# Kernel tuning notes

Hardware: AMD Instinct MI355X
Metric: run time of the kernel (lower is better)

The kernel has to match this reference:

```python
import jax, jax.numpy as jnp
import numpy as np

D = 256; FF = 1024; NH = 8; NL = 4; NP = 4; HD = D // NH
BS = 4; NQ = 300; NK = 17; LQ = NQ * NK
SHAPES = np.array([[92, 92], [46, 46], [23, 23], [12, 12]], dtype=np.int32)  # (H, W) per level
LV = int((SHAPES[:, 0] * SHAPES[:, 1]).sum())  # 11253

PKEYS = ['wa_in_w','wa_in_b','wa_out_w','wa_out_b','ac_in_w','ac_in_b','ac_out_w','ac_out_b',
         'ms_val_w','ms_val_b','ms_off_w','ms_off_b','ms_aw_w','ms_aw_b','ms_out_w','ms_out_b',
         'gate_w','gate_b','gn_g','gn_b','wn_g','wn_b','an_g','an_b',
         'l1_w','l1_b','l2_w','l2_b','n2_g','n2_b']

def _ln(x, g, b, eps=1e-5):
    m = x.mean(-1, keepdims=True)
    v = ((x - m) ** 2).mean(-1, keepdims=True)
    return (x - m) / jnp.sqrt(v + eps) * g + b

def _mha(q, k, v, in_w, in_b, out_w, out_b):
    # torch nn.MultiheadAttention (batch_first) equivalent
    B, L, _ = q.shape
    wq, wk, wv = jnp.split(in_w, 3, 0); bq, bk, bv = jnp.split(in_b, 3, 0)
    qh = (q @ wq.T + bq).reshape(B, L, NH, HD).transpose(0, 2, 1, 3)
    kh = (k @ wk.T + bk).reshape(B, -1, NH, HD).transpose(0, 2, 1, 3)
    vh = (v @ wv.T + bv).reshape(B, -1, NH, HD).transpose(0, 2, 1, 3)
    scores = jnp.einsum('bhqd,bhkd->bhqk', qh, kh) / jnp.sqrt(jnp.asarray(HD, qh.dtype))
    a = jax.nn.softmax(scores, axis=-1)
    o = jnp.einsum('bhqk,bhkd->bhqd', a, vh).transpose(0, 2, 1, 3).reshape(B, L, D)
    return o @ out_w.T + out_b

def _bilinear(v, loc):
    # v: (bs,H,W,NH,HD); loc: (bs,Lq,NH,P,2) normalized [0,1]. grid_sample bilinear,
    # align_corners=False, zero padding.
    bs, H, W, nh, hd = v.shape
    x = loc[..., 0] * W - 0.5
    y = loc[..., 1] * H - 0.5
    x0 = jnp.floor(x); y0 = jnp.floor(y)
    wx = x - x0; wy = y - y0
    x0i = x0.astype(jnp.int32); y0i = y0.astype(jnp.int32)
    v_flat = v.reshape(bs, H * W, nh, hd)
    Lq, P = loc.shape[1], loc.shape[3]
    def corner(xi, yi):
        valid = ((xi >= 0) & (xi < W) & (yi >= 0) & (yi < H)).astype(v.dtype)
        idx = jnp.clip(yi, 0, H - 1) * W + jnp.clip(xi, 0, W - 1)  # (bs,Lq,NH,P)
        idx2 = idx.transpose(0, 1, 3, 2).reshape(bs, Lq * P, nh)
        g = jnp.take_along_axis(v_flat, idx2[..., None], axis=1)  # (bs,Lq*P,NH,HD)
        g = g.reshape(bs, Lq, P, nh, hd).transpose(0, 1, 3, 2, 4)
        return g * valid[..., None]
    v00 = corner(x0i, y0i); v01 = corner(x0i + 1, y0i)
    v10 = corner(x0i, y0i + 1); v11 = corner(x0i + 1, y0i + 1)
    return (v00 * ((1 - wx) * (1 - wy))[..., None] + v01 * (wx * (1 - wy))[..., None]
            + v10 * ((1 - wx) * wy)[..., None] + v11 * (wx * wy)[..., None])

def _msda(query, ref, memory, p):
    # standard MSDeformAttn core (fused sample + weight)
    bs, Lq, _ = query.shape
    val = (memory @ p['ms_val_w'].T + p['ms_val_b']).reshape(bs, -1, NH, HD)
    off = (query @ p['ms_off_w'].T + p['ms_off_b']).reshape(bs, Lq, NH, NL, NP, 2)
    aw = jax.nn.softmax((query @ p['ms_aw_w'].T + p['ms_aw_b']).reshape(bs, Lq, NH, NL * NP), -1)
    aw = aw.reshape(bs, Lq, NH, NL, NP)
    norm = jnp.asarray(SHAPES[:, ::-1].copy(), query.dtype)  # (NL,2) -> (W,H)
    loc = ref[:, :, None, :, None, :] + off / norm[None, None, None, :, None, :]
    out = jnp.zeros((bs, Lq, NH, HD), query.dtype)
    start = 0
    for l in range(NL):
        H, W = int(SHAPES[l, 0]), int(SHAPES[l, 1])
        vlev = val[:, start:start + H * W].reshape(bs, H, W, NH, HD); start += H * W
        s = _bilinear(vlev, loc[:, :, :, l])  # (bs,Lq,NH,NP,HD)
        out = out + (s * aw[:, :, :, l, :, None]).sum(3)
    return out.reshape(bs, Lq, D) @ p['ms_out_w'].T + p['ms_out_b']

def _forward(tgt_pose, pos, ref, memory, p):
    bs, nq, nk, d = tgt_pose.shape
    # with_pos_embed mutates tgt_pose in-place in the torch code
    tgt_pose = tgt_pose + pos
    q = tgt_pose.reshape(bs * nq, nk, d)
    t2 = _mha(q, q, q, p['wa_in_w'], p['wa_in_b'], p['wa_out_w'], p['wa_out_b']).reshape(bs, nq, nk, d)
    tgt_pose = _ln(tgt_pose + t2, p['wn_g'], p['wn_b'])
    t = tgt_pose.transpose(0, 2, 1, 3).reshape(bs * nk, nq, d)
    t2 = _mha(t, t, t, p['ac_in_w'], p['ac_in_b'], p['ac_out_w'], p['ac_out_b'])
    t = _ln(t + t2, p['an_g'], p['an_b'])
    tgt_pose = t.reshape(bs, nk, nq, d).transpose(0, 2, 1, 3)
    tgt_pose = tgt_pose + pos  # in-place with_pos_embed before cross attn
    t2 = _msda(tgt_pose.reshape(bs, nq * nk, d), ref, memory, p).reshape(bs, nq, nk, d)
    gi = jnp.concatenate([tgt_pose, t2], -1)
    gates = jax.nn.sigmoid(gi @ p['gate_w'].T + p['gate_b'])
    g1, g2 = jnp.split(gates, 2, -1)
    x = _ln(g1 * tgt_pose + g2 * t2, p['gn_g'], p['gn_b'])
    f = jax.nn.relu(x @ p['l1_w'].T + p['l1_b']) @ p['l2_w'].T + p['l2_b']
    return _ln(x + f, p['n2_g'], p['n2_b'])

def setup_inputs() -> dict:
    key = jax.random.key(0)
    ks = iter(jax.random.split(key, 64))
    s = 0.02
    inp = {
        'tgt_pose': jax.random.normal(next(ks), (BS, NQ, NK, D), jnp.float32),
        'tgt_pose_query_pos': jax.random.normal(next(ks), (BS, NQ, NK, D), jnp.float32),
        'tgt_pose_reference_points': jax.random.uniform(next(ks), (BS, LQ, NL, 2), jnp.float32),
        'memory': jax.random.normal(next(ks), (BS, LV, D), jnp.float32),
        'memory_spatial_shapes': jnp.asarray(SHAPES),
    }
    shapes = {
        'wa_in_w': (3 * D, D), 'wa_in_b': (3 * D,), 'wa_out_w': (D, D), 'wa_out_b': (D,),
        'ac_in_w': (3 * D, D), 'ac_in_b': (3 * D,), 'ac_out_w': (D, D), 'ac_out_b': (D,),
        'ms_val_w': (D, D), 'ms_val_b': (D,),
        'ms_off_w': (NH * NL * NP * 2, D), 'ms_off_b': (NH * NL * NP * 2,),
        'ms_aw_w': (NH * NL * NP, D), 'ms_aw_b': (NH * NL * NP,),
        'ms_out_w': (D, D), 'ms_out_b': (D,),
        'gate_w': (2 * D, 2 * D), 'gate_b': (2 * D,),
        'l1_w': (FF, D), 'l1_b': (FF,), 'l2_w': (D, FF), 'l2_b': (D,),
    }
    for k, sh in shapes.items():
        inp[k] = jax.random.normal(next(ks), sh, jnp.float32) * s
    for k in ['gn_g', 'wn_g', 'an_g', 'n2_g']:
        inp[k] = jnp.ones((D,), jnp.float32)
    for k in ['gn_b', 'wn_b', 'an_b', 'n2_b']:
        inp[k] = jnp.zeros((D,), jnp.float32)
    return inp

def reference(tgt_pose, tgt_pose_query_pos, tgt_pose_reference_points, memory, memory_spatial_shapes,
              wa_in_w, wa_in_b, wa_out_w, wa_out_b, ac_in_w, ac_in_b, ac_out_w, ac_out_b,
              ms_val_w, ms_val_b, ms_off_w, ms_off_b, ms_aw_w, ms_aw_b, ms_out_w, ms_out_b,
              gate_w, gate_b, gn_g, gn_b, wn_g, wn_b, an_g, an_b,
              l1_w, l1_b, l2_w, l2_b, n2_g, n2_b):
    p = dict(wa_in_w=wa_in_w, wa_in_b=wa_in_b, wa_out_w=wa_out_w, wa_out_b=wa_out_b,
             ac_in_w=ac_in_w, ac_in_b=ac_in_b, ac_out_w=ac_out_w, ac_out_b=ac_out_b,
             ms_val_w=ms_val_w, ms_val_b=ms_val_b, ms_off_w=ms_off_w, ms_off_b=ms_off_b,
             ms_aw_w=ms_aw_w, ms_aw_b=ms_aw_b, ms_out_w=ms_out_w, ms_out_b=ms_out_b,
             gate_w=gate_w, gate_b=gate_b, gn_g=gn_g, gn_b=gn_b, wn_g=wn_g, wn_b=wn_b,
             an_g=an_g, an_b=an_b, l1_w=l1_w, l1_b=l1_b, l2_w=l2_w, l2_b=l2_b, n2_g=n2_g, n2_b=n2_b)
    return _forward(tgt_pose, tgt_pose_query_pos, tgt_pose_reference_points, memory, p)
```

## Files before the change

### kernel.cpp

```cpp
#include <hip/hip_runtime.h>
#include <math.h>

#define DD   256
#define NHH  8
#define HDIM 32
#define NLV  4
#define NPT  4
#define BSZ  4
#define NQQ  300
#define NKK  17
#define LQQ  (NQQ*NKK)
#define NROW (BSZ*LQQ)
#define LVV  11253
#define FFD  1024

typedef __attribute__((ext_vector_type(8))) short bf16x8;
typedef __attribute__((ext_vector_type(4))) float f32x4;

__device__ __forceinline__ unsigned short f2bf(float f) {
    unsigned int u = __float_as_uint(f);
    u = u + 0x7FFFu + ((u >> 16) & 1u);
    return (unsigned short)(u >> 16);
}

__global__ __launch_bounds__(256) void k_add(const float4* __restrict__ a,
                                             const float4* __restrict__ b,
                                             float4* __restrict__ o, int n4) {
    int i = blockIdx.x * 256 + threadIdx.x;
    if (i < n4) {
        float4 x = a[i], y = b[i];
        o[i] = make_float4(x.x + y.x, x.y + y.y, x.z + y.z, x.w + y.w);
    }
}

__global__ __launch_bounds__(256) void k_concat(const float4* __restrict__ a,
                                                const float4* __restrict__ b,
                                                float4* __restrict__ o, int rows) {
    int i = blockIdx.x * 256 + threadIdx.x;
    if (i >= rows * 128) return;
    int r = i >> 7, c = i & 127;
    o[i] = (c < 64) ? a[(size_t)r * 64 + c] : b[(size_t)r * 64 + (c - 64)];
}

template<int ACT>
__global__ __launch_bounds__(256) void k_gemm_mfma(const float* __restrict__ A,
                                                   const float* __restrict__ B,
                                                   const float* __restrict__ bias,
                                                   float* __restrict__ C,
                                                   int M, int N, int K) {
    __shared__ unsigned short As[128][40];
    __shared__ unsigned short Bs[128][40];
    int t = threadIdx.x;
    int lane = t & 63, w = t >> 6;
    int l16 = lane & 15, hi = lane >> 4;
    int wr = (w >> 1) << 6;
    int wc = (w & 1) << 6;
    int row0 = blockIdx.x * 128, col0 = blockIdx.y * 128;
    int srow = t >> 2;
    int scol = (t & 3) * 8;

    f32x4 acc[4][4];
    #pragma unroll
    for (int m = 0; m < 4; m++)
        #pragma unroll
        for (int n = 0; n < 4; n++) acc[m][n] = (f32x4){0.f, 0.f, 0.f, 0.f};

    for (int k0 = 0; k0 < K; k0 += 32) {
        #pragma unroll
        for (int half = 0; half < 2; half++) {
            int r = srow + half * 64;
            {
                float v[8];
                int gr = row0 + r;
                if (gr < M) {
                    const float4* p = (const float4*)(A + (size_t)gr * K + k0 + scol);
                    float4 x = p[0], y = p[1];
                    v[0] = x.x; v[1] = x.y; v[2] = x.z; v[3] = x.w;
                    v[4] = y.x; v[5] = y.y; v[6] = y.z; v[7] = y.w;
                } else {
                    #pragma unroll
                    for (int i = 0; i < 8; i++) v[i] = 0.f;
                }
                bf16x8 hh;
                #pragma unroll
                for (int i = 0; i < 8; i++) hh[i] = (short)f2bf(v[i]);
                *(bf16x8*)&As[r][scol] = hh;
            }
            {
                int gb = col0 + r;
                const float4* p = (const float4*)(B + (size_t)gb * K + k0 + scol);
                float4 x = p[0], y = p[1];
                float v[8] = {x.x, x.y, x.z, x.w, y.x, y.y, y.z, y.w};
                bf16x8 hh;
                #pragma unroll
                for (int i = 0; i < 8; i++) hh[i] = (short)f2bf(v[i]);
                *(bf16x8*)&Bs[r][scol] = hh;
            }
        }
        __syncthreads();
        bf16x8 af[4], bfr[4];
        #pragma unroll
        for (int m = 0; m < 4; m++) af[m] = *(const bf16x8*)&As[wr + m * 16 + l16][hi * 8];
        #pragma unroll
        for (int n = 0; n < 4; n++) bfr[n] = *(const bf16x8*)&Bs[wc + n * 16 + l16][hi * 8];
        #pragma unroll
        for (int m = 0; m < 4; m++)
            #pragma unroll
            for (int n = 0; n < 4; n++)
                acc[m][n] = __builtin_amdgcn_mfma_f32_16x16x32_bf16(af[m], bfr[n], acc[m][n], 0, 0, 0);
        __syncthreads();
    }
    #pragma unroll
    for (int n = 0; n < 4; n++) {
        int col = col0 + wc + n * 16 + l16;
        float bv = bias[col];
        #pragma unroll
        for (int m = 0; m < 4; m++) {
            #pragma unroll
            for (int r = 0; r < 4; r++) {
                int row = row0 + wr + m * 16 + (hi << 2) + r;
                if (row < M) {
                    float v = acc[m][n][r] + bv;
                    if (ACT == 1) v = fmaxf(v, 0.f);
                    else if (ACT == 2) v = 1.f / (1.f + __expf(-v));
                    C[(size_t)row * N + col] = v;
                }
            }
        }
    }
}

__global__ __launch_bounds__(256) void k_ln_res(const float* __restrict__ A,
                                                const float* __restrict__ Bp,
                                                const float* __restrict__ g,
                                                const float* __restrict__ be,
                                                float* __restrict__ O, int M) {
    int row = blockIdx.x * 4 + (threadIdx.x >> 6);
    int lane = threadIdx.x & 63;
    if (row >= M) return;
    float4 a = ((const float4*)A)[(size_t)row * 64 + lane];
    float4 b = ((const float4*)Bp)[(size_t)row * 64 + lane];
    float x0 = a.x + b.x, x1 = a.y + b.y, x2 = a.z + b.z, x3 = a.w + b.w;
    float s = x0 + x1 + x2 + x3;
    float sq = x0 * x0 + x1 * x1 + x2 * x2 + x3 * x3;
    #pragma unroll
    for (int o = 32; o; o >>= 1) { s += __shfl_xor(s, o); sq += __shfl_xor(sq, o); }
    float mean = s * (1.f / 256.f);
    float var = sq * (1.f / 256.f) - mean * mean;
    float rs = rsqrtf(var + 1e-5f);
    float4 gg = ((const float4*)g)[lane];
    float4 bb = ((const float4*)be)[lane];
    float4 o4;
    o4.x = (x0 - mean) * rs * gg.x + bb.x;
    o4.y = (x1 - mean) * rs * gg.y + bb.y;
    o4.z = (x2 - mean) * rs * gg.z + bb.z;
    o4.w = (x3 - mean) * rs * gg.w + bb.w;
    ((float4*)O)[(size_t)row * 64 + lane] = o4;
}

__global__ __launch_bounds__(256) void k_ln_gate(const float* __restrict__ G,
                                                 const float* __restrict__ Q,
                                                 const float* __restrict__ T2,
                                                 const float* __restrict__ g,
                                                 const float* __restrict__ be,
                                                 float* __restrict__ O, int M) {
    int row = blockIdx.x * 4 + (threadIdx.x >> 6);
    int lane = threadIdx.x & 63;
    if (row >= M) return;
    float4 g1 = ((const float4*)G)[(size_t)row * 128 + lane];
    float4 g2 = ((const float4*)G)[(size_t)row * 128 + 64 + lane];
    float4 q = ((const float4*)Q)[(size_t)row * 64 + lane];
    float4 t = ((const float4*)T2)[(size_t)row * 64 + lane];
    float x0 = g1.x * q.x + g2.x * t.x;
    float x1 = g1.y * q.y + g2.y * t.y;
    float x2 = g1.z * q.z + g2.z * t.z;
    float x3 = g1.w * q.w + g2.w * t.w;
    float s = x0 + x1 + x2 + x3;
    float sq = x0 * x0 + x1 * x1 + x2 * x2 + x3 * x3;
    #pragma unroll
    for (int o = 32; o; o >>= 1) { s += __shfl_xor(s, o); sq += __shfl_xor(sq, o); }
    float mean = s * (1.f / 256.f);
    float var = sq * (1.f / 256.f) - mean * mean;
    float rs = rsqrtf(var + 1e-5f);
    float4 gg = ((const float4*)g)[lane];
    float4 bb = ((const float4*)be)[lane];
    float4 o4;
    o4.x = (x0 - mean) * rs * gg.x + bb.x;
    o4.y = (x1 - mean) * rs * gg.y + bb.y;
    o4.z = (x2 - mean) * rs * gg.z + bb.z;
    o4.w = (x3 - mean) * rs * gg.w + bb.w;
    ((float4*)O)[(size_t)row * 64 + lane] = o4;
}

__global__ __launch_bounds__(64) void k_wattn(const float* __restrict__ QKV,
                                              float* __restrict__ AO) {
    int unit = blockIdx.x;
    int h = unit & 7;
    int sqc = unit >> 3;
    int lane = threadIdx.x;
    __shared__ float q[17][32], kk[17][32], vv[17][32], sc[17][17];
    for (int idx = lane; idx < 17 * 32; idx += 64) {
        int r = idx >> 5, c = idx & 31;
        const float* base = QKV + (size_t)(sqc * 17 + r) * 768 + h * 32 + c;
        q[r][c] = base[0];
        kk[r][c] = base[256];
        vv[r][c] = base[512];
    }
    __syncthreads();
    const float scale = 0.17677669529663687f;
    for (int idx = lane; idx < 289; idx += 64) {
        int i = idx / 17, j = idx % 17;
        float d = 0.f;
        #pragma unroll
        for (int c = 0; c < 32; c++) d += q[i][c] * kk[j][c];
        sc[i][j] = d * scale;
    }
    __syncthreads();
    if (lane < 17) {
        float mm = -1e30f;
        for (int j = 0; j < 17; j++) mm = fmaxf(mm, sc[lane][j]);
        float ss = 0.f;
        for (int j = 0; j < 17; j++) { float e = __expf(sc[lane][j] - mm); sc[lane][j] = e; ss += e; }
        float iv = 1.f / ss;
        for (int j = 0; j < 17; j++) sc[lane][j] *= iv;
    }
    __syncthreads();
    for (int idx = lane; idx < 17 * 32; idx += 64) {
        int i = idx >> 5, c = idx & 31;
        float o = 0.f;
        #pragma unroll
        for (int j = 0; j < 17; j++) o += sc[i][j] * vv[j][c];
        AO[(size_t)(sqc * 17 + i) * 256 + h * 32 + c] = o;
    }
}

__global__ __launch_bounds__(256) void k_acattn_mfma(const float* __restrict__ QKV,
                                                     float* __restrict__ AO) {
    __shared__ unsigned short Ks[64][40];
    __shared__ unsigned short Vt[32][66];
    __shared__ unsigned short Pl[4][16][72];

    int blk = blockIdx.x;
    int qb = blk % 5;
    int rest = blk / 5;
    int h = rest & 7;
    int bk = rest >> 3;
    int kslot = bk % 17;
    int b = bk / 17;

    int t = threadIdx.x;
    int lane = t & 63, w = t >> 6;
    int l16 = lane & 15, hi = lane >> 4;
    const float scale = 0.17677669529663687f;

    int q0 = qb * 64;
    int qrow = q0 + (w << 4) + l16;
    int qc = qrow < 300 ? qrow : 299;
    bf16x8 qf;
    {
        const float* qp = QKV + ((size_t)(b * 300 + qc) * 17 + kslot) * 768 + h * 32 + hi * 8;
        float4 x = ((const float4*)qp)[0];
        float4 y = ((const float4*)qp)[1];
        float v[8] = {x.x, x.y, x.z, x.w, y.x, y.y, y.z, y.w};
        #pragma unroll
        for (int i = 0; i < 8; i++) qf[i] = (short)f2bf(v[i] * scale);
    }

    f32x4 acc0 = (f32x4){0.f, 0.f, 0.f, 0.f};
    f32x4 acc1 = (f32x4){0.f, 0.f, 0.f, 0.f};
    float m[4], l[4];
    #pragma unroll
    for (int r = 0; r < 4; r++) { m[r] = -1e30f; l[r] = 0.f; }

    int jl = t >> 2;
    int sc = (t & 3) * 8;

    for (int c0 = 0; c0 < 300; c0 += 64) {
        __syncthreads();
        {
            int krow = c0 + jl; if (krow > 299) krow = 299;
            const float* kp = QKV + ((size_t)(b * 300 + krow) * 17 + kslot) * 768 + 256 + h * 32 + sc;
            float4 x = ((const float4*)kp)[0];
            float4 y = ((const float4*)kp)[1];
            float v[8] = {x.x, x.y, x.z, x.w, y.x, y.y, y.z, y.w};
            bf16x8 hK;
            #pragma unroll
            for (int i = 0; i < 8; i++) hK[i] = (short)f2bf(v[i]);
            *(bf16x8*)&Ks[jl][sc] = hK;
            const float* vp = kp + 256;
            float4 vx = ((const float4*)vp)[0];
            float4 vy = ((const float4*)vp)[1];
            float vv[8] = {vx.x, vx.y, vx.z, vx.w, vy.x, vy.y, vy.z, vy.w};
            #pragma unroll
            for (int i = 0; i < 8; i++) Vt[sc + i][jl] = f2bf(vv[i]);
        }
        __syncthreads();

        f32x4 S[4];
        #pragma unroll
        for (int jt = 0; jt < 4; jt++) {
            bf16x8 kf = *(const bf16x8*)&Ks[jt * 16 + l16][hi * 8];
            S[jt] = __builtin_amdgcn_mfma_f32_16x16x32_bf16(qf, kf,
                     (f32x4){0.f, 0.f, 0.f, 0.f}, 0, 0, 0);
        }
        float cm[4] = {-1e30f, -1e30f, -1e30f, -1e30f};
        #pragma unroll
        for (int jt = 0; jt < 4; jt++) {
            bool ok = (c0 + jt * 16 + l16) < 300;
            #pragma unroll
            for (int r = 0; r < 4; r++) {
                float s = ok ? S[jt][r] : -1e30f;
                S[jt][r] = s;
                cm[r] = fmaxf(cm[r], s);
            }
        }
        #pragma unroll
        for (int o = 1; o < 16; o <<= 1)
            #pragma unroll
            for (int r = 0; r < 4; r++) cm[r] = fmaxf(cm[r], __shfl_xor(cm[r], o));
        float corr[4];
        #pragma unroll
        for (int r = 0; r < 4; r++) {
            float nm = fmaxf(m[r], cm[r]);
            corr[r] = __expf(m[r] - nm);
            m[r] = nm;
        }
        float ps[4] = {0.f, 0.f, 0.f, 0.f};
        #pragma unroll
        for (int jt = 0; jt < 4; jt++)
            #pragma unroll
            for (int r = 0; r < 4; r++) {
                float p = __expf(S[jt][r] - m[r]);
                S[jt][r] = p;
                ps[r] += p;
            }
        #pragma unroll
        for (int o = 1; o < 16; o <<= 1)
            #pragma unroll
            for (int r = 0; r < 4; r++) ps[r] += __shfl_xor(ps[r], o);
        #pragma unroll
        for (int r = 0; r < 4; r++) l[r] = l[r] * corr[r] + ps[r];
        #pragma unroll
        for (int r = 0; r < 4; r++) { acc0[r] *= corr[r]; acc1[r] *= corr[r]; }
        #pragma unroll
        for (int jt = 0; jt < 4; jt++)
            #pragma unroll
            for (int r = 0; r < 4; r++)
                Pl[w][(hi << 2) + r][jt * 16 + l16] = f2bf(S[jt][r]);
        #pragma unroll
        for (int half = 0; half < 2; half++) {
            bf16x8 pf = *(const bf16x8*)&Pl[w][l16][half * 32 + hi * 8];
            bf16x8 vf0 = *(const bf16x8*)&Vt[l16][half * 32 + hi * 8];
            bf16x8 vf1 = *(const bf16x8*)&Vt[16 + l16][half * 32 + hi * 8];
            acc0 = __builtin_amdgcn_mfma_f32_16x16x32_bf16(pf, vf0, acc0, 0, 0, 0);
            acc1 = __builtin_amdgcn_mfma_f32_16x16x32_bf16(pf, vf1, acc1, 0, 0, 0);
        }
    }
    #pragma unroll
    for (int r = 0; r < 4; r++) {
        int q = q0 + (w << 4) + (hi << 2) + r;
        if (q < 300) {
            float inv = 1.f / l[r];
            float* op = AO + ((size_t)(b * 300 + q) * 17 + kslot) * 256 + h * 32;
            op[l16] = acc0[r] * inv;
            op[16 + l16] = acc1[r] * inv;
        }
    }
}

__global__ __launch_bounds__(256) void k_msda(const float* __restrict__ OFF,
                                              const float* __restrict__ AWL,
                                              const float* __restrict__ REF,
                                              const float* __restrict__ VAL,
                                              float* __restrict__ OUT) {
    __shared__ int   sIdx[128][4];
    __shared__ float sWgt[128][4];
    const int Hs[4] = {92, 46, 23, 12};
    const int starts[4] = {0, 8464, 10580, 11109};
    int rowq = blockIdx.x;
    int b = rowq / 5100;
    int tid = threadIdx.x;

    if (tid < 128) {
        int h = tid >> 4, p = tid & 15;
        float logit = AWL[(size_t)rowq * 128 + h * 16 + p];
        float mx = logit;
        #pragma unroll
        for (int o = 1; o < 16; o <<= 1) mx = fmaxf(mx, __shfl_xor(mx, o));
        float e = __expf(logit - mx);
        float ssum = e;
        #pragma unroll
        for (int o = 1; o < 16; o <<= 1) ssum += __shfl_xor(ssum, o);
        float aw = e / ssum;

        int l = p >> 2;
        int Ww = Hs[l];
        float fw = (float)Ww;
        float rx = REF[(size_t)rowq * 8 + l * 2];
        float ry = REF[(size_t)rowq * 8 + l * 2 + 1];
        float ox = OFF[(size_t)rowq * 256 + h * 32 + p * 2];
        float oy = OFF[(size_t)rowq * 256 + h * 32 + p * 2 + 1];
        float x = (rx + ox / fw) * fw - 0.5f;
        float y = (ry + oy / fw) * fw - 0.5f;
        float x0f = floorf(x), y0f = floorf(y);
        float wx = x - x0f, wy = y - y0f;
        int x0 = (int)x0f, y0 = (int)y0f;
        bool xv0 = (x0 >= 0) & (x0 < Ww), xv1 = (x0 + 1 >= 0) & (x0 + 1 < Ww);
        bool yv0 = (y0 >= 0) & (y0 < Ww), yv1 = (y0 + 1 >= 0) & (y0 + 1 < Ww);
        int x0c = min(max(x0, 0), Ww - 1), x1c = min(max(x0 + 1, 0), Ww - 1);
        int y0c = min(max(y0, 0), Ww - 1), y1c = min(max(y0 + 1, 0), Ww - 1);
        int base = b * LVV + starts[l];
        sIdx[tid][0] = base + y0c * Ww + x0c;
        sIdx[tid][1] = base + y0c * Ww + x1c;
        sIdx[tid][2] = base + y1c * Ww + x0c;
        sIdx[tid][3] = base + y1c * Ww + x1c;
        sWgt[tid][0] = (yv0 && xv0) ? (1.f - wx) * (1.f - wy) * aw : 0.f;
        sWgt[tid][1] = (yv0 && xv1) ? wx * (1.f - wy) * aw : 0.f;
        sWgt[tid][2] = (yv1 && xv0) ? (1.f - wx) * wy * aw : 0.f;
        sWgt[tid][3] = (yv1 && xv1) ? wx * wy * aw : 0.f;
    }
    __syncthreads();

    int h = tid >> 5, hd = tid & 31;
    int off = h * 32 + hd;
    float out = 0.f;
    #pragma unroll
    for (int p = 0; p < 16; p++) {
        int mI = h * 16 + p;
        int i0 = sIdx[mI][0], i1 = sIdx[mI][1], i2 = sIdx[mI][2], i3 = sIdx[mI][3];
        float w0 = sWgt[mI][0], w1 = sWgt[mI][1], w2 = sWgt[mI][2], w3 = sWgt[mI][3];
        out += w0 * VAL[(size_t)i0 * 256 + off]
             + w1 * VAL[(size_t)i1 * 256 + off]
             + w2 * VAL[(size_t)i2 * 256 + off]
             + w3 * VAL[(size_t)i3 * 256 + off];
    }
    OUT[(size_t)rowq * 256 + off] = out;
}

extern "C" void kernel_launch(void* const* d_in, const int* in_sizes, int n_in,
                              void* d_out, int out_size, void* d_ws, size_t ws_size,
                              hipStream_t stream) {
    const float* tgt     = (const float*)d_in[0];
    const float* pos     = (const float*)d_in[1];
    const float* refpts  = (const float*)d_in[2];
    const float* memory  = (const float*)d_in[3];
    const float* wa_in_w  = (const float*)d_in[5];
    const float* wa_in_b  = (const float*)d_in[6];
    const float* wa_out_w = (const float*)d_in[7];
    const float* wa_out_b = (const float*)d_in[8];
    const float* ac_in_w  = (const float*)d_in[9];
    const float* ac_in_b  = (const float*)d_in[10];
    const float* ac_out_w = (const float*)d_in[11];
    const float* ac_out_b = (const float*)d_in[12];
    const float* ms_val_w = (const float*)d_in[13];
    const float* ms_val_b = (const float*)d_in[14];
    const float* ms_off_w = (const float*)d_in[15];
    const float* ms_off_b = (const float*)d_in[16];
    const float* ms_aw_w  = (const float*)d_in[17];
    const float* ms_aw_b  = (const float*)d_in[18];
    const float* ms_out_w = (const float*)d_in[19];
    const float* ms_out_b = (const float*)d_in[20];
    const float* gate_w   = (const float*)d_in[21];
    const float* gate_b   = (const float*)d_in[22];
    const float* l1_w     = (const float*)d_in[23];
    const float* l1_b     = (const float*)d_in[24];
    const float* l2_w     = (const float*)d_in[25];
    const float* l2_b     = (const float*)d_in[26];
    const float* gn_g     = (const float*)d_in[27];
    const float* wn_g     = (const float*)d_in[28];
    const float* an_g     = (const float*)d_in[29];
    const float* n2_g     = (const float*)d_in[30];
    const float* gn_b     = (const float*)d_in[31];
    const float* wn_b     = (const float*)d_in[32];
    const float* an_b     = (const float*)d_in[33];
    const float* n2_b     = (const float*)d_in[34];

    float* ws = (float*)d_ws;
    const size_t SROW = (size_t)NROW * 256;
    float* TP  = ws;
    float* Qb  = ws + SROW;
    float* T2  = ws + 2 * SROW;
    float* BIG = ws + 3 * SROW;
    float* OFF = BIG;
    float* AW  = BIG + SROW;
    float* VAL = BIG + (size_t)NROW * 384;
    float* GI    = BIG;
    float* GATES = BIG + (size_t)NROW * 512;
    float* Xb  = (float*)d_out;

    const int n4 = NROW * 64;
    const int gx = (NROW + 127) / 128;
    const int gxv = (BSZ * LVV + 127) / 128;

    k_add<<<(n4 + 255) / 256, 256, 0, stream>>>((const float4*)tgt, (const float4*)pos, (float4*)TP, n4);
    k_gemm_mfma<0><<<dim3(gx, 6), 256, 0, stream>>>(TP, wa_in_w, wa_in_b, BIG, NROW, 768, 256);
    k_wattn<<<1200 * 8, 64, 0, stream>>>(BIG, T2);
    k_gemm_mfma<0><<<dim3(gx, 2), 256, 0, stream>>>(T2, wa_out_w, wa_out_b, Xb, NROW, 256, 256);
    k_ln_res<<<(NROW + 3) / 4, 256, 0, stream>>>(TP, Xb, wn_g, wn_b, TP, NROW);
    k_gemm_mfma<0><<<dim3(gx, 6), 256, 0, stream>>>(TP, ac_in_w, ac_in_b, BIG, NROW, 768, 256);
    k_acattn_mfma<<<68 * 8 * 5, 256, 0, stream>>>(BIG, T2);
    k_gemm_mfma<0><<<dim3(gx, 2), 256, 0, stream>>>(T2, ac_out_w, ac_out_b, Xb, NROW, 256, 256);
    k_ln_res<<<(NROW + 3) / 4, 256, 0, stream>>>(TP, Xb, an_g, an_b, TP, NROW);
    k_add<<<(n4 + 255) / 256, 256, 0, stream>>>((const float4*)TP, (const float4*)pos, (float4*)Qb, n4);
    k_gemm_mfma<0><<<dim3(gxv, 2), 256, 0, stream>>>(memory, ms_val_w, ms_val_b, VAL, BSZ * LVV, 256, 256);
    k_gemm_mfma<0><<<dim3(gx, 2), 256, 0, stream>>>(Qb, ms_off_w, ms_off_b, OFF, NROW, 256, 256);
    k_gemm_mfma<0><<<dim3(gx, 1), 256, 0, stream>>>(Qb, ms_aw_w, ms_aw_b, AW, NROW, 128, 256);
    k_msda<<<NROW, 256, 0, stream>>>(OFF, AW, refpts, VAL, TP);
    k_gemm_mfma<0><<<dim3(gx, 2), 256, 0, stream>>>(TP, ms_out_w, ms_out_b, T2, NROW, 256, 256);
    k_concat<<<(NROW * 128 + 255) / 256, 256, 0, stream>>>((const float4*)Qb, (const float4*)T2, (float4*)GI, NROW);
    k_gemm_mfma<2><<<dim3(gx, 4), 256, 0, stream>>>(GI, gate_w, gate_b, GATES, NROW, 512, 512);
    k_ln_gate<<<(NROW + 3) / 4, 256, 0, stream>>>(GATES, Qb, T2, gn_g, gn_b, Xb, NROW);
    k_gemm_mfma<1><<<dim3(gx, 8), 256, 0, stream>>>(Xb, l1_w, l1_b, BIG, NROW, 1024, 256);
    k_gemm_mfma<0><<<dim3(gx, 2), 256, 0, stream>>>(BIG, l2_w, l2_b, T2, NROW, 256, 1024);
    k_ln_res<<<(NROW + 3) / 4, 256, 0, stream>>>(Xb, T2, n2_g, n2_b, (float*)d_out, NROW);
}
```

Baseline: 838.7 us.

## Store intermediate activations and weights in bf16 across the pipeline

Pre-converts all weight matrices to bf16 once per call and switches most intermediate activation buffers (QKV, attention outputs, offsets, values, gates, FFN hidden) to bf16. GEMMs now load bf16 operands directly and can emit bf16 and/or fp32 outputs, and the attention, MSDA and gate-LN kernels read bf16 inputs. This roughly halves memory traffic for intermediates and removes per-tile conversion work inside GEMMs, at the cost of extra rounding of intermediates and a weight conversion kernel per launch.

```diff
diff --git a/kernel.cpp b/kernel.cpp
--- a/kernel.cpp
+++ b/kernel.cpp
@@ -4,17 +4,15 @@
 #define DD   256
 #define NHH  8
 #define HDIM 32
-#define NLV  4
-#define NPT  4
 #define BSZ  4
 #define NQQ  300
 #define NKK  17
 #define LQQ  (NQQ*NKK)
 #define NROW (BSZ*LQQ)
 #define LVV  11253
-#define FFD  1024
 
 typedef __attribute__((ext_vector_type(8))) short bf16x8;
+typedef __attribute__((ext_vector_type(4))) short b16x4;
 typedef __attribute__((ext_vector_type(4))) float f32x4;
 
 __device__ __forceinline__ unsigned short f2bf(float f) {
@@ -22,39 +20,90 @@
     u = u + 0x7FFFu + ((u >> 16) & 1u);
     return (unsigned short)(u >> 16);
 }
-
-__global__ __launch_bounds__(256) void k_add(const float4* __restrict__ a,
-                                             const float4* __restrict__ b,
-                                             float4* __restrict__ o, int n4) {
+__device__ __forceinline__ float b2f(unsigned short u) {
+    return __uint_as_float((unsigned int)u << 16);
+}
+
+__global__ __launch_bounds__(256) void k_wcvt(const float* __restrict__ wa_in, const float* __restrict__ wa_out,
+                                              const float* __restrict__ ac_in, const float* __restrict__ ac_out,
+                                              const float* __restrict__ ms_val, const float* __restrict__ ms_off,
+                                              const float* __restrict__ ms_aw, const float* __restrict__ ms_out,
+                                              const float* __restrict__ gate, const float* __restrict__ l1,
+                                              const float* __restrict__ l2, unsigned short* __restrict__ W16) {
+    size_t idx = ((size_t)blockIdx.x * 256 + threadIdx.x) * 8;
+    if (idx >= 1540096) return;
+    const float* src; size_t loc;
+    if      (idx <  196608) { src = wa_in;  loc = idx; }
+    else if (idx <  262144) { src = wa_out; loc = idx -  196608; }
+    else if (idx <  458752) { src = ac_in;  loc = idx -  262144; }
+    else if (idx <  524288) { src = ac_out; loc = idx -  458752; }
+    else if (idx <  589824) { src = ms_val; loc = idx -  524288; }
+    else if (idx <  655360) { src = ms_off; loc = idx -  589824; }
+    else if (idx <  688128) { src = ms_aw;  loc = idx -  655360; }
+    else if (idx <  753664) { src = ms_out; loc = idx -  688128; }
+    else if (idx < 1015808) { src = gate;   loc = idx -  753664; }
+    else if (idx < 1277952) { src = l1;     loc = idx - 1015808; }
+    else                    { src = l2;     loc = idx - 1277952; }
+    float4 x = ((const float4*)(src + loc))[0];
+    float4 y = ((const float4*)(src + loc))[1];
+    float v[8] = {x.x, x.y, x.z, x.w, y.x, y.y, y.z, y.w};
+    bf16x8 h;
+    #pragma unroll
+    for (int i = 0; i < 8; i++) h[i] = (short)f2bf(v[i]);
+    *(bf16x8*)(W16 + idx) = h;
+}
+
+__global__ __launch_bounds__(256) void k_add_dw(const float4* __restrict__ a, const float4* __restrict__ b,
+                                                float4* __restrict__ o32, unsigned short* __restrict__ o16, int n8) {
     int i = blockIdx.x * 256 + threadIdx.x;
-    if (i < n4) {
-        float4 x = a[i], y = b[i];
-        o[i] = make_float4(x.x + y.x, x.y + y.y, x.z + y.z, x.w + y.w);
-    }
-}
-
-__global__ __launch_bounds__(256) void k_concat(const float4* __restrict__ a,
-                                                const float4* __restrict__ b,
-                                                float4* __restrict__ o, int rows) {
+    if (i >= n8) return;
+    float4 x0 = a[i * 2], y0 = b[i * 2];
+    float4 x1 = a[i * 2 + 1], y1 = b[i * 2 + 1];
+    float4 s0 = make_float4(x0.x + y0.x, x0.y + y0.y, x0.z + y0.z, x0.w + y0.w);
+    float4 s1 = make_float4(x1.x + y1.x, x1.y + y1.y, x1.z + y1.z, x1.w + y1.w);
+    o32[i * 2] = s0; o32[i * 2 + 1] = s1;
+    bf16x8 h;
+    h[0]=(short)f2bf(s0.x); h[1]=(short)f2bf(s0.y); h[2]=(short)f2bf(s0.z); h[3]=(short)f2bf(s0.w);
+    h[4]=(short)f2bf(s1.x); h[5]=(short)f2bf(s1.y); h[6]=(short)f2bf(s1.z); h[7]=(short)f2bf(s1.w);
+    *(bf16x8*)(o16 + (size_t)i * 8) = h;
+}
+
+__global__ __launch_bounds__(256) void k_add_b16(const float4* __restrict__ a, const float4* __restrict__ b,
+                                                 unsigned short* __restrict__ o16, int n8) {
     int i = blockIdx.x * 256 + threadIdx.x;
-    if (i >= rows * 128) return;
-    int r = i >> 7, c = i & 127;
-    o[i] = (c < 64) ? a[(size_t)r * 64 + c] : b[(size_t)r * 64 + (c - 64)];
-}
-
-template<int ACT>
-__global__ __launch_bounds__(256) void k_gemm_mfma(const float* __restrict__ A,
-                                                   const float* __restrict__ B,
+    if (i >= n8) return;
+    float4 x0 = a[i * 2], y0 = b[i * 2];
+    float4 x1 = a[i * 2 + 1], y1 = b[i * 2 + 1];
+    bf16x8 h;
+    h[0]=(short)f2bf(x0.x+y0.x); h[1]=(short)f2bf(x0.y+y0.y); h[2]=(short)f2bf(x0.z+y0.z); h[3]=(short)f2bf(x0.w+y0.w);
+    h[4]=(short)f2bf(x1.x+y1.x); h[5]=(short)f2bf(x1.y+y1.y); h[6]=(short)f2bf(x1.z+y1.z); h[7]=(short)f2bf(x1.w+y1.w);
+    *(bf16x8*)(o16 + (size_t)i * 8) = h;
+}
+
+__global__ __launch_bounds__(256) void k_concat16(const unsigned short* __restrict__ a,
+                                                  const unsigned short* __restrict__ b,
+                                                  unsigned short* __restrict__ o, int rows) {
+    int i = blockIdx.x * 256 + threadIdx.x;
+    if (i >= rows * 64) return;
+    int r = i >> 6, c8 = i & 63;
+    const unsigned short* src = (c8 < 32) ? (a + (size_t)r * 256 + c8 * 8)
+                                          : (b + (size_t)r * 256 + (c8 - 32) * 8);
+    *(bf16x8*)(o + (size_t)r * 512 + c8 * 8) = *(const bf16x8*)src;
+}
+
+template<int ACT, int OMODE, bool A32>
+__global__ __launch_bounds__(256) void k_gemm_mfma(const void* __restrict__ Av,
+                                                   const unsigned short* __restrict__ B,
                                                    const float* __restrict__ bias,
-                                                   float* __restrict__ C,
+                                                   float* __restrict__ C32,
+                                                   unsigned short* __restrict__ C16,
                                                    int M, int N, int K) {
     __shared__ unsigned short As[128][40];
     __shared__ unsigned short Bs[128][40];
     int t = threadIdx.x;
     int lane = t & 63, w = t >> 6;
     int l16 = lane & 15, hi = lane >> 4;
-    int wr = (w >> 1) << 6;
-    int wc = (w & 1) << 6;
+    int wr = (w >> 1) << 6, wc = (w & 1) << 6;
     int row0 = blockIdx.x * 128, col0 = blockIdx.y * 128;
     int srow = t >> 2;
     int scol = (t & 3) * 8;
@@ -69,14 +118,14 @@
         #pragma unroll
         for (int half = 0; half < 2; half++) {
             int r = srow + half * 64;
-            {
+            int gr = row0 + r;
+            if (A32) {
+                const float* A = (const float*)Av;
                 float v[8];
-                int gr = row0 + r;
                 if (gr < M) {
                     const float4* p = (const float4*)(A + (size_t)gr * K + k0 + scol);
                     float4 x = p[0], y = p[1];
-                    v[0] = x.x; v[1] = x.y; v[2] = x.z; v[3] = x.w;
-                    v[4] = y.x; v[5] = y.y; v[6] = y.z; v[7] = y.w;
+                    v[0]=x.x; v[1]=x.y; v[2]=x.z; v[3]=x.w; v[4]=y.x; v[5]=y.y; v[6]=y.z; v[7]=y.w;
                 } else {
                     #pragma unroll
                     for (int i = 0; i < 8; i++) v[i] = 0.f;
@@ -85,17 +134,15 @@
                 #pragma unroll
                 for (int i = 0; i < 8; i++) hh[i] = (short)f2bf(v[i]);
                 *(bf16x8*)&As[r][scol] = hh;
+            } else {
+                const unsigned short* A = (const unsigned short*)Av;
+                bf16x8 hh;
+                if (gr < M) hh = *(const bf16x8*)(A + (size_t)gr * K + k0 + scol);
+                else        hh = (bf16x8){0,0,0,0,0,0,0,0};
+                *(bf16x8*)&As[r][scol] = hh;
             }
-            {
-                int gb = col0 + r;
-                const float4* p = (const float4*)(B + (size_t)gb * K + k0 + scol);
-                float4 x = p[0], y = p[1];
-                float v[8] = {x.x, x.y, x.z, x.w, y.x, y.y, y.z, y.w};
-                bf16x8 hh;
-                #pragma unroll
-                for (int i = 0; i < 8; i++) hh[i] = (short)f2bf(v[i]);
-                *(bf16x8*)&Bs[r][scol] = hh;
-            }
+            int gb = col0 + r;
+            *(bf16x8*)&Bs[r][scol] = *(const bf16x8*)(B + (size_t)gb * K + k0 + scol);
         }
         __syncthreads();
         bf16x8 af[4], bfr[4];
@@ -123,18 +170,21 @@
                     float v = acc[m][n][r] + bv;
                     if (ACT == 1) v = fmaxf(v, 0.f);
                     else if (ACT == 2) v = 1.f / (1.f + __expf(-v));
-                    C[(size_t)row * N + col] = v;
+                    if (OMODE & 1) C32[(size_t)row * N + col] = v;
+                    if (OMODE & 2) C16[(size_t)row * N + col] = f2bf(v);
                 }
             }
         }
     }
 }
 
+template<bool DUAL>
 __global__ __launch_bounds__(256) void k_ln_res(const float* __restrict__ A,
                                                 const float* __restrict__ Bp,
                                                 const float* __restrict__ g,
                                                 const float* __restrict__ be,
-                                                float* __restrict__ O, int M) {
+                                                float* __restrict__ O,
+                                                unsigned short* __restrict__ O16, int M) {
     int row = blockIdx.x * 4 + (threadIdx.x >> 6);
     int lane = threadIdx.x & 63;
     if (row >= M) return;
@@ -156,25 +206,31 @@
     o4.z = (x2 - mean) * rs * gg.z + bb.z;
     o4.w = (x3 - mean) * rs * gg.w + bb.w;
     ((float4*)O)[(size_t)row * 64 + lane] = o4;
-}
-
-__global__ __launch_bounds__(256) void k_ln_gate(const float* __restrict__ G,
-                                                 const float* __restrict__ Q,
-                                                 const float* __restrict__ T2,
-                                                 const float* __restrict__ g,
-                                                 const float* __restrict__ be,
-                                                 float* __restrict__ O, int M) {
+    if (DUAL) {
+        b16x4 h;
+        h[0]=(short)f2bf(o4.x); h[1]=(short)f2bf(o4.y); h[2]=(short)f2bf(o4.z); h[3]=(short)f2bf(o4.w);
+        *(b16x4*)(O16 + (size_t)row * 256 + lane * 4) = h;
+    }
+}
+
+__global__ __launch_bounds__(256) void k_ln_gate_b(const unsigned short* __restrict__ G,
+                                                   const unsigned short* __restrict__ Q,
+                                                   const unsigned short* __restrict__ T2,
+                                                   const float* __restrict__ g,
+                                                   const float* __restrict__ be,
+                                                   float* __restrict__ O,
+                                                   unsigned short* __restrict__ O16, int M) {
     int row = blockIdx.x * 4 + (threadIdx.x >> 6);
     int lane = threadIdx.x & 63;
     if (row >= M) return;
-    float4 g1 = ((const float4*)G)[(size_t)row * 128 + lane];
-    float4 g2 = ((const float4*)G)[(size_t)row * 128 + 64 + lane];
-    float4 q = ((const float4*)Q)[(size_t)row * 64 + lane];
-    float4 t = ((const float4*)T2)[(size_t)row * 64 + lane];
-    float x0 = g1.x * q.x + g2.x * t.x;
-    float x1 = g1.y * q.y + g2.y * t.y;
-    float x2 = g1.z * q.z + g2.z * t.z;
-    float x3 = g1.w * q.w + g2.w * t.w;
+    b16x4 g1 = *(const b16x4*)(G + (size_t)row * 512 + lane * 4);
+    b16x4 g2 = *(const b16x4*)(G + (size_t)row * 512 + 256 + lane * 4);
+    b16x4 q  = *(const b16x4*)(Q + (size_t)row * 256 + lane * 4);
+    b16x4 tt = *(const b16x4*)(T2 + (size_t)row * 256 + lane * 4);
+    float x0 = b2f((unsigned short)g1[0]) * b2f((unsigned short)q[0]) + b2f((unsigned short)g2[0]) * b2f((unsigned short)tt[0]);
+    float x1 = b2f((unsigned short)g1[1]) * b2f((unsigned short)q[1]) + b2f((unsigned short)g2[1]) * b2f((unsigned short)tt[1]);
+    float x2 = b2f((unsigned short)g1[2]) * b2f((unsigned short)q[2]) + b2f((unsigned short)g2[2]) * b2f((unsigned short)tt[2]);
+    float x3 = b2f((unsigned short)g1[3]) * b2f((unsigned short)q[3]) + b2f((unsigned short)g2[3]) * b2f((unsigned short)tt[3]);
     float s = x0 + x1 + x2 + x3;
     float sq = x0 * x0 + x1 * x1 + x2 * x2 + x3 * x3;
     #pragma unroll
@@ -190,10 +246,13 @@
     o4.z = (x2 - mean) * rs * gg.z + bb.z;
     o4.w = (x3 - mean) * rs * gg.w + bb.w;
     ((float4*)O)[(size_t)row * 64 + lane] = o4;
-}
-
-__global__ __launch_bounds__(64) void k_wattn(const float* __restrict__ QKV,
-                                              float* __restrict__ AO) {
+    b16x4 h;
+    h[0]=(short)f2bf(o4.x); h[1]=(short)f2bf(o4.y); h[2]=(short)f2bf(o4.z); h[3]=(short)f2bf(o4.w);
+    *(b16x4*)(O16 + (size_t)row * 256 + lane * 4) = h;
+}
+
+__global__ __launch_bounds__(64) void k_wattn_b(const unsigned short* __restrict__ QKV,
+                                                unsigned short* __restrict__ AO) {
     int unit = blockIdx.x;
     int h = unit & 7;
     int sqc = unit >> 3;
@@ -201,10 +260,10 @@
     __shared__ float q[17][32], kk[17][32], vv[17][32], sc[17][17];
     for (int idx = lane; idx < 17 * 32; idx += 64) {
         int r = idx >> 5, c = idx & 31;
-        const float* base = QKV + (size_t)(sqc * 17 + r) * 768 + h * 32 + c;
-        q[r][c] = base[0];
-        kk[r][c] = base[256];
-        vv[r][c] = base[512];
+        const unsigned short* base = QKV + (size_t)(sqc * 17 + r) * 768 + h * 32 + c;
+        q[r][c] = b2f(base[0]);
+        kk[r][c] = b2f(base[256]);
+        vv[r][c] = b2f(base[512]);
     }
     __syncthreads();
     const float scale = 0.17677669529663687f;
@@ -230,12 +289,12 @@
         float o = 0.f;
         #pragma unroll
         for (int j = 0; j < 17; j++) o += sc[i][j] * vv[j][c];
-        AO[(size_t)(sqc * 17 + i) * 256 + h * 32 + c] = o;
-    }
-}
-
-__global__ __launch_bounds__(256) void k_acattn_mfma(const float* __restrict__ QKV,
-                                                     float* __restrict__ AO) {
+        AO[(size_t)(sqc * 17 + i) * 256 + h * 32 + c] = f2bf(o);
+    }
+}
+
+__global__ __launch_bounds__(256) void k_acattn_mfma_b(const unsigned short* __restrict__ QKV,
+                                                       unsigned short* __restrict__ AO) {
     __shared__ unsigned short Ks[64][40];
     __shared__ unsigned short Vt[32][66];
     __shared__ unsigned short Pl[4][16][72];
@@ -256,15 +315,7 @@
     int q0 = qb * 64;
     int qrow = q0 + (w << 4) + l16;
     int qc = qrow < 300 ? qrow : 299;
-    bf16x8 qf;
-    {
-        const float* qp = QKV + ((size_t)(b * 300 + qc) * 17 + kslot) * 768 + h * 32 + hi * 8;
-        float4 x = ((const float4*)qp)[0];
-        float4 y = ((const float4*)qp)[1];
-        float v[8] = {x.x, x.y, x.z, x.w, y.x, y.y, y.z, y.w};
-        #pragma unroll
-        for (int i = 0; i < 8; i++) qf[i] = (short)f2bf(v[i] * scale);
-    }
+    bf16x8 qf = *(const bf16x8*)(QKV + ((size_t)(b * 300 + qc) * 17 + kslot) * 768 + h * 32 + hi * 8);
 
     f32x4 acc0 = (f32x4){0.f, 0.f, 0.f, 0.f};
     f32x4 acc1 = (f32x4){0.f, 0.f, 0.f, 0.f};
@@ -279,20 +330,11 @@
         __syncthreads();
         {
             int krow = c0 + jl; if (krow > 299) krow = 299;
-            const float* kp = QKV + ((size_t)(b * 300 + krow) * 17 + kslot) * 768 + 256 + h * 32 + sc;
-            float4 x = ((const float4*)kp)[0];
-            float4 y = ((const float4*)kp)[1];
-            float v[8] = {x.x, x.y, x.z, x.w, y.x, y.y, y.z, y.w};
-            bf16x8 hK;
-            #pragma unroll
-            for (int i = 0; i < 8; i++) hK[i] = (short)f2bf(v[i]);
-            *(bf16x8*)&Ks[jl][sc] = hK;
-            const float* vp = kp + 256;
-            float4 vx = ((const float4*)vp)[0];
-            float4 vy = ((const float4*)vp)[1];
-            float vv[8] = {vx.x, vx.y, vx.z, vx.w, vy.x, vy.y, vy.z, vy.w};
-            #pragma unroll
-            for (int i = 0; i < 8; i++) Vt[sc + i][jl] = f2bf(vv[i]);
+            const unsigned short* kp = QKV + ((size_t)(b * 300 + krow) * 17 + kslot) * 768 + 256 + h * 32 + sc;
+            *(bf16x8*)&Ks[jl][sc] = *(const bf16x8*)kp;
+            bf16x8 vv = *(const bf16x8*)(kp + 256);
+            #pragma unroll
+            for (int i = 0; i < 8; i++) Vt[sc + i][jl] = (unsigned short)vv[i];
         }
         __syncthreads();
 
@@ -309,7 +351,7 @@
             bool ok = (c0 + jt * 16 + l16) < 300;
             #pragma unroll
             for (int r = 0; r < 4; r++) {
-                float s = ok ? S[jt][r] : -1e30f;
+                float s = ok ? S[jt][r] * scale : -1e30f;
                 S[jt][r] = s;
                 cm[r] = fmaxf(cm[r], s);
             }
@@ -361,18 +403,18 @@
         int q = q0 + (w << 4) + (hi << 2) + r;
         if (q < 300) {
             float inv = 1.f / l[r];
-            float* op = AO + ((size_t)(b * 300 + q) * 17 + kslot) * 256 + h * 32;
-            op[l16] = acc0[r] * inv;
-            op[16 + l16] = acc1[r] * inv;
-        }
-    }
-}
-
-__global__ __launch_bounds__(256) void k_msda(const float* __restrict__ OFF,
-                                              const float* __restrict__ AWL,
-                                              const float* __restrict__ REF,
-                                              const float* __restrict__ VAL,
-                                              float* __restrict__ OUT) {
+            unsigned short* op = AO + ((size_t)(b * 300 + q) * 17 + kslot) * 256 + h * 32;
+            op[l16] = f2bf(acc0[r] * inv);
+            op[16 + l16] = f2bf(acc1[r] * inv);
+        }
+    }
+}
+
+__global__ __launch_bounds__(256) void k_msda_b(const unsigned short* __restrict__ OFF,
+                                                const unsigned short* __restrict__ AWL,
+                                                const float* __restrict__ REF,
+                                                const unsigned short* __restrict__ VAL,
+                                                unsigned short* __restrict__ OUT) {
     __shared__ int   sIdx[128][4];
     __shared__ float sWgt[128][4];
     const int Hs[4] = {92, 46, 23, 12};
@@ -383,7 +425,7 @@
 
     if (tid < 128) {
         int h = tid >> 4, p = tid & 15;
-        float logit = AWL[(size_t)rowq * 128 + h * 16 + p];
+        float logit = b2f(AWL[(size_t)rowq * 128 + h * 16 + p]);
         float mx = logit;
         #pragma unroll
         for (int o = 1; o < 16; o <<= 1) mx = fmaxf(mx, __shfl_xor(mx, o));
@@ -398,8 +440,8 @@
         float fw = (float)Ww;
         float rx = REF[(size_t)rowq * 8 + l * 2];
         float ry = REF[(size_t)rowq * 8 + l * 2 + 1];
-        float ox = OFF[(size_t)rowq * 256 + h * 32 + p * 2];
-        float oy = OFF[(size_t)rowq * 256 + h * 32 + p * 2 + 1];
+        float ox = b2f(OFF[(size_t)rowq * 256 + h * 32 + p * 2]);
+        float oy = b2f(OFF[(size_t)rowq * 256 + h * 32 + p * 2 + 1]);
         float x = (rx + ox / fw) * fw - 0.5f;
         float y = (ry + oy / fw) * fw - 0.5f;
         float x0f = floorf(x), y0f = floorf(y);
@@ -429,12 +471,12 @@
         int mI = h * 16 + p;
         int i0 = sIdx[mI][0], i1 = sIdx[mI][1], i2 = sIdx[mI][2], i3 = sIdx[mI][3];
         float w0 = sWgt[mI][0], w1 = sWgt[mI][1], w2 = sWgt[mI][2], w3 = sWgt[mI][3];
-        out += w0 * VAL[(size_t)i0 * 256 + off]
-             + w1 * VAL[(size_t)i1 * 256 + off]
-             + w2 * VAL[(size_t)i2 * 256 + off]
-             + w3 * VAL[(size_t)i3 * 256 + off];
-    }
-    OUT[(size_t)rowq * 256 + off] = out;
+        out += w0 * b2f(VAL[(size_t)i0 * 256 + off])
+             + w1 * b2f(VAL[(size_t)i1 * 256 + off])
+             + w2 * b2f(VAL[(size_t)i2 * 256 + off])
+             + w3 * b2f(VAL[(size_t)i3 * 256 + off]);
+    }
+    OUT[(size_t)rowq * 256 + off] = f2bf(out);
 }
 
 extern "C" void kernel_launch(void* const* d_in, const int* in_sizes, int n_in,
@@ -475,42 +517,63 @@
     const float* an_b     = (const float*)d_in[33];
     const float* n2_b     = (const float*)d_in[34];
 
-    float* ws = (float*)d_ws;
-    const size_t SROW = (size_t)NROW * 256;
-    float* TP  = ws;
-    float* Qb  = ws + SROW;
-    float* T2  = ws + 2 * SROW;
-    float* BIG = ws + 3 * SROW;
-    float* OFF = BIG;
-    float* AW  = BIG + SROW;
-    float* VAL = BIG + (size_t)NROW * 384;
-    float* GI    = BIG;
-    float* GATES = BIG + (size_t)NROW * 512;
-    float* Xb  = (float*)d_out;
-
-    const int n4 = NROW * 64;
+    const size_t SROWF = (size_t)NROW * 256;
+    float* TP32 = (float*)d_ws;
+    float* T232 = TP32 + SROWF;
+    unsigned short* us0 = (unsigned short*)(TP32 + 2 * SROWF);
+    unsigned short* OFF16 = us0;
+    unsigned short* AW16  = us0 + 5222400;
+    unsigned short* TP16  = us0 + 7833600;
+    unsigned short* T216  = us0 + 13056000;
+    unsigned short* Qb16  = us0 + 18278400;
+    unsigned short* X16   = us0 + 23500800;
+    unsigned short* W16   = us0 + 28723200;
+    unsigned short* SH    = us0 + 30263296;
+    unsigned short* QKV16  = SH;
+    unsigned short* VAL16  = SH;
+    unsigned short* MS16   = SH + 12000000;
+    unsigned short* GI16   = SH;
+    unsigned short* GATES16= SH + 10444800;
+    unsigned short* F116   = SH;
+    float* Xb32 = (float*)d_out;
+
+    const unsigned short* W_wa_in  = W16;
+    const unsigned short* W_wa_out = W16 + 196608;
+    const unsigned short* W_ac_in  = W16 + 262144;
+    const unsigned short* W_ac_out = W16 + 458752;
+    const unsigned short* W_ms_val = W16 + 524288;
+    const unsigned short* W_ms_off = W16 + 589824;
+    const unsigned short* W_ms_aw  = W16 + 655360;
+    const unsigned short* W_ms_out = W16 + 688128;
+    const unsigned short* W_gate   = W16 + 753664;
+    const unsigned short* W_l1     = W16 + 1015808;
+    const unsigned short* W_l2     = W16 + 1277952;
+
+    const int n8 = NROW * 32;
     const int gx = (NROW + 127) / 128;
     const int gxv = (BSZ * LVV + 127) / 128;
 
-    k_add<<<(n4 + 255) / 256, 256, 0, stream>>>((const float4*)tgt, (const float4*)pos, (float4*)TP, n4);
-    k_gemm_mfma<0><<<dim3(gx, 6), 256, 0, stream>>>(TP, wa_in_w, wa_in_b, BIG, NROW, 768, 256);
-    k_wattn<<<1200 * 8, 64, 0, stream>>>(BIG, T2);
-    k_gemm_mfma<0><<<dim3(gx, 2), 256, 0, stream>>>(T2, wa_out_w, wa_out_b, Xb, NROW, 256, 256);
-    k_ln_res<<<(NROW + 3) / 4, 256, 0, stream>>>(TP, Xb, wn_g, wn_b, TP, NROW);
-    k_gemm_mfma<0><<<dim3(gx, 6), 256, 0, stream>>>(TP, ac_in_w, ac_in_b, BIG, NROW, 768, 256);
-    k_acattn_mfma<<<68 * 8 * 5, 256, 0, stream>>>(BIG, T2);
-    k_gemm_mfma<0><<<dim3(gx, 2), 256, 0, stream>>>(T2, ac_out_w, ac_out_b, Xb, NROW, 256, 256);
-    k_ln_res<<<(NROW + 3) / 4, 256, 0, stream>>>(TP, Xb, an_g, an_b, TP, NROW);
-    k_add<<<(n4 + 255) / 256, 256, 0, stream>>>((const float4*)TP, (const float4*)pos, (float4*)Qb, n4);
-    k_gemm_mfma<0><<<dim3(gxv, 2), 256, 0, stream>>>(memory, ms_val_w, ms_val_b, VAL, BSZ * LVV, 256, 256);
-    k_gemm_mfma<0><<<dim3(gx, 2), 256, 0, stream>>>(Qb, ms_off_w, ms_off_b, OFF, NROW, 256, 256);
-    k_gemm_mfma<0><<<dim3(gx, 1), 256, 0, stream>>>(Qb, ms_aw_w, ms_aw_b, AW, NROW, 128, 256);
-    k_msda<<<NROW, 256, 0, stream>>>(OFF, AW, refpts, VAL, TP);
-    k_gemm_mfma<0><<<dim3(gx, 2), 256, 0, stream>>>(TP, ms_out_w, ms_out_b, T2, NROW, 256, 256);
-    k_concat<<<(NROW * 128 + 255) / 256, 256, 0, stream>>>((const float4*)Qb, (const float4*)T2, (float4*)GI, NROW);
-    k_gemm_mfma<2><<<dim3(gx, 4), 256, 0, stream>>>(GI, gate_w, gate_b, GATES, NROW, 512, 512);
-    k_ln_gate<<<(NROW + 3) / 4, 256, 0, stream>>>(GATES, Qb, T2, gn_g, gn_b, Xb, NROW);
-    k_gemm_mfma<1><<<dim3(gx, 8), 256, 0, stream>>>(Xb, l1_w, l1_b, BIG, NROW, 1024, 256);
-    k_gemm_mfma<0><<<dim3(gx, 2), 256, 0, stream>>>(BIG, l2_w, l2_b, T2, NROW, 256, 1024);
-    k_ln_res<<<(NROW + 3) / 4, 256, 0, stream>>>(Xb, T2, n2_g, n2_b, (float*)d_out, NROW);
-}
+    k_wcvt<<<753, 256, 0, stream>>>(wa_in_w, wa_out_w, ac_in_w, ac_out_w, ms_val_w, ms_off_w,
+                                    ms_aw_w, ms_out_w, gate_w, l1_w, l2_w, W16);
+    k_add_dw<<<(n8 + 255) / 256, 256, 0, stream>>>((const float4*)tgt, (const float4*)pos, (float4*)TP32, TP16, n8);
+    k_gemm_mfma<0, 2, false><<<dim3(gx, 6), 256, 0, stream>>>(TP16, W_wa_in, wa_in_b, nullptr, QKV16, NROW, 768, 256);
+    k_wattn_b<<<1200 * 8, 64, 0, stream>>>(QKV16, T216);
+    k_gemm_mfma<0, 1, false><<<dim3(gx, 2), 256, 0, stream>>>(T216, W_wa_out, wa_out_b, Xb32, nullptr, NROW, 256, 256);
+    k_ln_res<true><<<(NROW + 3) / 4, 256, 0, stream>>>(TP32, Xb32, wn_g, wn_b, TP32, TP16, NROW);
+    k_gemm_mfma<0, 2, false><<<dim3(gx, 6), 256, 0, stream>>>(TP16, W_ac_in, ac_in_b, nullptr, QKV16, NROW, 768, 256);
+    k_acattn_mfma_b<<<68 * 8 * 5, 256, 0, stream>>>(QKV16, T216);
+    k_gemm_mfma<0, 1, false><<<dim3(gx, 2), 256, 0, stream>>>(T216, W_ac_out, ac_out_b, Xb32, nullptr, NROW, 256, 256);
+    k_ln_res<false><<<(NROW + 3) / 4, 256, 0, stream>>>(TP32, Xb32, an_g, an_b, TP32, nullptr, NROW);
+    k_add_b16<<<(n8 + 255) / 256, 256, 0, stream>>>((const float4*)TP32, (const float4*)pos, Qb16, n8);
+    k_gemm_mfma<0, 2, true><<<dim3(gxv, 2), 256, 0, stream>>>(memory, W_ms_val, ms_val_b, nullptr, VAL16, BSZ * LVV, 256, 256);
+    k_gemm_mfma<0, 2, false><<<dim3(gx, 2), 256, 0, stream>>>(Qb16, W_ms_off, ms_off_b, nullptr, OFF16, NROW, 256, 256);
+    k_gemm_mfma<0, 2, false><<<dim3(gx, 1), 256, 0, stream>>>(Qb16, W_ms_aw, ms_aw_b, nullptr, AW16, NROW, 128, 256);
+    k_msda_b<<<NROW, 256, 0, stream>>>(OFF16, AW16, refpts, VAL16, MS16);
+    k_gemm_mfma<0, 2, false><<<dim3(gx, 2), 256, 0, stream>>>(MS16, W_ms_out, ms_out_b, nullptr, T216, NROW, 256, 256);
+    k_concat16<<<(NROW * 64 + 255) / 256, 256, 0, stream>>>(Qb16, T216, GI16, NROW);
+    k_gemm_mfma<2, 2, false><<<dim3(gx, 4), 256, 0, stream>>>(GI16, W_gate, gate_b, nullptr, GATES16, NROW, 512, 512);
+    k_ln_gate_b<<<(NROW + 3) / 4, 256, 0, stream>>>(GATES16, Qb16, T216, gn_g, gn_b, Xb32, X16, NROW);
+    k_gemm_mfma<1, 2, false><<<dim3(gx, 8), 256, 0, stream>>>(X16, W_l1, l1_b, nullptr, F116, NROW, 1024, 256);
+    k_gemm_mfma<0, 1, false><<<dim3(gx, 2), 256, 0, stream>>>(F116, W_l2, l2_b, T232, nullptr, NROW, 256, 1024);
+    k_ln_res<false><<<(NROW + 3) / 4, 256, 0, stream>>>(Xb32, T232, n2_g, n2_b, (float*)d_out, nullptr, NROW);
+}
```

After: 681.7 us. -18.7%, faster.
